# Kernel tuning notes

Measured on AMD Instinct MI355X. Metric: run time of the kernel, lower is better.

The kernel has to match this reference:

```python
import jax, jax.numpy as jnp
import numpy as np

B, H, W, C = 2, 128, 128, 256
WS = 8            # current_window (query window)
KW = 16           # halo_window = 2*current_window
HEADS = 8
HD = C // HEADS
PRETRAIN = 8
CPB_HIDDEN = 512


def _rel_bias_consts():
    halo = (KW - WS) // 2
    coords = np.arange(1 - WS - halo, WS + halo, dtype=np.float32)  # length WS+KW-1 = 23
    tab = np.stack(np.meshgrid(coords, coords, indexing='ij'), axis=-1)  # [23,23,2]
    tab = tab * (8.0 / (PRETRAIN - 1.0))
    tab = np.sign(tab) * np.log1p(np.abs(tab)) / np.log(8.0)
    tab = tab.reshape(-1, 2).astype(np.float32)                      # [529,2]
    qi = np.arange(WS)
    qg = np.stack(np.meshgrid(qi, qi, indexing='ij')).reshape(2, -1)  # [2,64]
    ki = np.arange(KW)
    kg = np.stack(np.meshgrid(ki, ki, indexing='ij')).reshape(2, -1)  # [2,256]
    rel = qg[:, :, None] - kg[:, None] + (KW - 1)
    idx = (rel[0] * (WS + KW - 1) + rel[1]).reshape(-1).astype(np.int32)  # [64*256]
    return tab, idx

_REL_TAB, _REL_IDX = _rel_bias_consts()


def setup_inputs() -> dict:
    key = jax.random.key(0)
    ks = jax.random.split(key, 12)
    s = 0.02
    return {
        'x': jax.random.normal(ks[0], (B, H, W, C), jnp.float32),
        'w_qkv': jax.random.normal(ks[1], (C, 3 * C), jnp.float32) * s,
        'w_dw': jax.random.normal(ks[2], (3, 3, 1, 3 * C), jnp.float32) * s,  # depthwise HWIO
        'ln_g': jnp.ones((3 * C,), jnp.float32),
        'ln_b': jnp.zeros((3 * C,), jnp.float32),
        'q_bias': jnp.zeros((C,), jnp.float32),
        'v_bias': jnp.zeros((C,), jnp.float32),
        'logit_scale': jnp.full((HEADS, 1, 1), np.log(10.0), jnp.float32),
        'cpb_w1': jax.random.normal(ks[3], (2, CPB_HIDDEN), jnp.float32) * s,
        'cpb_b1': jnp.zeros((CPB_HIDDEN,), jnp.float32),
        'cpb_w2': jax.random.normal(ks[4], (CPB_HIDDEN, HEADS), jnp.float32) * s,
        'w_proj': jax.random.normal(ks[5], (C, C), jnp.float32) * s,
    }


def _l2n(t):
    # tf.math.l2_normalize with epsilon=1.55e-5
    return t * jax.lax.rsqrt(jnp.maximum(jnp.sum(t * t, -1, keepdims=True), 1.55e-5))


def reference(x, w_qkv, w_dw, ln_g, ln_b, q_bias, v_bias, logit_scale,
              cpb_w1, cpb_b1, cpb_w2, w_proj):
    nWh, nWw = H // WS, W // WS
    nW = nWh * nWw
    # qkv 1x1 conv + depthwise 3x3 + layernorm + (q,0,v) bias
    qkv = jnp.einsum('bhwc,cd->bhwd', x, w_qkv)
    qkv = jax.lax.conv_general_dilated(
        qkv, w_dw, (1, 1), 'SAME',
        dimension_numbers=('NHWC', 'HWIO', 'NHWC'), feature_group_count=3 * C)
    mu = jnp.mean(qkv, -1, keepdims=True)
    var = jnp.var(qkv, -1, keepdims=True)
    qkv = (qkv - mu) * jax.lax.rsqrt(var + 1e-5) * ln_g + ln_b
    qkv = qkv + jnp.concatenate([q_bias, jnp.zeros_like(q_bias), v_bias])
    q, kv = qkv[..., :C], qkv[..., C:]
    # window partition of q: [B*nW, heads, WS*WS, HD]
    qp = q.reshape(B, nWh, WS, nWw, WS, HEADS, HD)
    qp = qp.transpose(0, 1, 3, 5, 2, 4, 6).reshape(B * nW, HEADS, WS * WS, HD)
    # halo partition of kv: overlapping KWxKW patches, stride WS
    halo = (KW - WS) // 2
    kvp = jnp.pad(kv, ((0, 0), (halo, halo), (halo, halo), (0, 0)))
    ridx = (np.arange(nWh) * WS)[:, None] + np.arange(KW)[None]  # [nWh,KW]
    cidx = (np.arange(nWw) * WS)[:, None] + np.arange(KW)[None]  # [nWw,KW]
    kvp = kvp[:, ridx][:, :, :, cidx]               # [B,nWh,KW,nWw,KW,2C]
    kvp = kvp.transpose(0, 1, 3, 2, 4, 5).reshape(B * nW, KW * KW, 2, HEADS, HD)
    k = kvp[:, :, 0].transpose(0, 2, 1, 3)          # [B*nW, heads, KW*KW, HD]
    v = kvp[:, :, 1].transpose(0, 2, 1, 3)
    # cosine attention with clamped learned log-scale
    scale = jnp.exp(jnp.minimum(logit_scale, np.float32(np.log(100.0))))
    attn = jnp.einsum('whqd,whkd->whqk', _l2n(qp) * scale, _l2n(k))
    # continuous relative position bias (CPB MLP + gather)
    hidden = jax.nn.relu(jnp.asarray(_REL_TAB) @ cpb_w1 + cpb_b1)
    bias_tab = jax.nn.sigmoid(hidden @ cpb_w2) * 16.0        # [529, heads]
    rb = bias_tab[_REL_IDX].reshape(WS * WS, KW * KW, HEADS).transpose(2, 0, 1)
    attn = jax.nn.softmax(attn + rb[None], axis=-1)
    out = jnp.einsum('whqk,whkd->whqd', attn, v)             # [B*nW, heads, 64, HD]
    # reverse window partition
    out = out.reshape(B, nWh, nWw, HEADS, WS, WS, HD)
    out = out.transpose(0, 1, 4, 2, 5, 3, 6).reshape(B, H, W, C)
    return jnp.einsum('bhwc,cd->bhwd', out, w_proj)
```

## Files before the change

kernel.cpp:

```cpp
#include <hip/hip_runtime.h>
#include <hip/hip_bf16.h>
#include <hip/hip_fp16.h>
#include <cstddef>
#include <cstdint>

#define BB 2
#define HH 128
#define WW 128
#define CC 256
#define WSZ 8
#define KWIN 16
#define NHEADS 8
#define HD 32
#define C3 768
#define NPIX 32768
#define NWIN 512

typedef short    bf16x8 __attribute__((ext_vector_type(8)));
typedef _Float16 half8  __attribute__((ext_vector_type(8)));
typedef float    f32x4  __attribute__((ext_vector_type(4)));

#define LOG2E 1.4426950408889634f

#if __has_builtin(__builtin_amdgcn_exp2f)
#define EXP2(x) __builtin_amdgcn_exp2f(x)
#else
#define EXP2(x) __expf((x) * 0.6931471805599453f)
#endif

__device__ inline void gload_lds16(const _Float16* g, _Float16* l) {
    __builtin_amdgcn_global_load_lds(
        (const __attribute__((address_space(1))) unsigned int*)g,
        (__attribute__((address_space(3))) unsigned int*)l, 16, 0, 0);
}

__global__ __launch_bounds__(64) void cpb_kernel(const float* __restrict__ w1,
                                                 const float* __restrict__ b1,
                                                 const float* __restrict__ w2,
                                                 float* __restrict__ btab) {
    const int e = blockIdx.x;
    const int i = e / 23, j = e % 23;
    const float inv_log8 = 1.0f / logf(8.0f);
    float c0 = (float)(i - 11) * (8.0f / 7.0f);
    float c1 = (float)(j - 11) * (8.0f / 7.0f);
    float f0 = copysignf(log1pf(fabsf(c0)) * inv_log8, c0);
    float f1 = copysignf(log1pf(fabsf(c1)) * inv_log8, c1);

    const int t = threadIdx.x;
    float acc[8] = {0.f,0.f,0.f,0.f,0.f,0.f,0.f,0.f};
    for (int kk = 0; kk < 8; kk++) {
        int k = kk * 64 + t;
        float hid = f0 * w1[k] + f1 * w1[512 + k] + b1[k];
        hid = fmaxf(hid, 0.f);
        #pragma unroll
        for (int h = 0; h < 8; h++) acc[h] += hid * w2[k * 8 + h];
    }
    #pragma unroll
    for (int h = 0; h < 8; h++) {
        #pragma unroll
        for (int off = 32; off >= 1; off >>= 1) acc[h] += __shfl_xor(acc[h], off);
    }
    if (t < 8) {
        float v = acc[t];
        btab[e * 8 + t] = 16.0f / (1.0f + expf(-v));
    }
}

__global__ __launch_bounds__(256) void cvt_wdw(const float* __restrict__ src,
                                               _Float16* __restrict__ dst) {
    int i = blockIdx.x * 256 + threadIdx.x;
    if (i < 9 * C3) dst[i] = (_Float16)src[i];
}

__global__ __launch_bounds__(256) void transpose_cvt(const float* __restrict__ src,
                                                     _Float16* __restrict__ dst,
                                                     int R, int Cn) {
    __shared__ float t[32][33];
    const int bx = blockIdx.x, by = blockIdx.y;
    const int tx = threadIdx.x & 31, ty = threadIdx.x >> 5;
    #pragma unroll
    for (int i = 0; i < 4; i++) {
        int r = by * 32 + ty + i * 8;
        t[ty + i * 8][tx] = src[(size_t)r * Cn + bx * 32 + tx];
    }
    __syncthreads();
    #pragma unroll
    for (int i = 0; i < 4; i++) {
        int dr = bx * 32 + ty + i * 8;
        dst[(size_t)dr * R + by * 32 + tx] = (_Float16)t[tx][ty + i * 8];
    }
}

template <typename OT>
__global__ __launch_bounds__(256) void gemm_f16(const _Float16* __restrict__ A,
                                                const _Float16* __restrict__ Bt,
                                                OT* __restrict__ C,
                                                int M, int N, int K) {
    __shared__ _Float16 Ash[128][64];
    __shared__ _Float16 Bsh[128][64];
    const int tid = threadIdx.x;
    const int wv = tid >> 6, ln = tid & 63;
    const int quad = ln >> 4, l15 = ln & 15;
    const int rowb = blockIdx.y * 128;
    const int colb = blockIdx.x * 128;
    const int wm = (wv >> 1) * 64, wn = (wv & 1) * 64;

    const int r8 = ln >> 3, g = ln & 7;
    const int kg = g ^ r8;

    f32x4 acc[4][4] = {};
    for (int k0 = 0; k0 < K; k0 += 64) {
        #pragma unroll
        for (int i = 0; i < 4; i++) {
            const int m = wv * 32 + i * 8 + r8;
            gload_lds16(A + (size_t)(rowb + m) * K + k0 + kg * 8,
                        &Ash[wv * 32 + i * 8][0]);
            gload_lds16(Bt + (size_t)(colb + m) * K + k0 + kg * 8,
                        &Bsh[wv * 32 + i * 8][0]);
        }
        __syncthreads();
        #pragma unroll
        for (int kk = 0; kk < 2; kk++) {
            const int phys = ((kk * 4 + quad) ^ (l15 & 7)) * 8;
            half8 a[4], b[4];
            #pragma unroll
            for (int i = 0; i < 4; i++)
                a[i] = *(const half8*)&Ash[wm + i * 16 + l15][phys];
            #pragma unroll
            for (int j = 0; j < 4; j++)
                b[j] = *(const half8*)&Bsh[wn + j * 16 + l15][phys];
            #pragma unroll
            for (int i = 0; i < 4; i++)
                #pragma unroll
                for (int j = 0; j < 4; j++)
                    acc[i][j] = __builtin_amdgcn_mfma_f32_16x16x32_f16(
                        a[i], b[j], acc[i][j], 0, 0, 0);
        }
        __syncthreads();
    }
    #pragma unroll
    for (int i = 0; i < 4; i++) {
        #pragma unroll
        for (int reg = 0; reg < 4; reg++) {
            const size_t row = rowb + wm + i * 16 + quad * 4 + reg;
            #pragma unroll
            for (int j = 0; j < 4; j++) {
                C[row * N + colb + wn + j * 16 + l15] = (OT)acc[i][j][reg];
            }
        }
    }
}

__global__ __launch_bounds__(256) void gemm_qkv(const float* __restrict__ A,
                                                const _Float16* __restrict__ Bt,
                                                _Float16* __restrict__ C,
                                                int M, int N, int K) {
    __shared__ _Float16 Ash[128][64];
    __shared__ _Float16 Bsh[128][64];
    const int tid = threadIdx.x;
    const int wv = tid >> 6, ln = tid & 63;
    const int quad = ln >> 4, l15 = ln & 15;
    const int rowb = blockIdx.y * 128;
    const int colb = blockIdx.x * 128;
    const int wm = (wv >> 1) * 64, wn = (wv & 1) * 64;
    const int r8 = ln >> 3, g = ln & 7;
    const int kg = g ^ r8;

    f32x4 acc[4][4] = {};
    for (int k0 = 0; k0 < K; k0 += 64) {
        #pragma unroll
        for (int i = 0; i < 4; i++) {
            const int m = wv * 32 + i * 8 + r8;
            const float* ap = A + (size_t)(rowb + m) * K + k0 + g * 8;
            const float4 a0 = *(const float4*)ap;
            const float4 a1 = *(const float4*)(ap + 4);
            half8 hv;
            hv[0] = (_Float16)a0.x; hv[1] = (_Float16)a0.y;
            hv[2] = (_Float16)a0.z; hv[3] = (_Float16)a0.w;
            hv[4] = (_Float16)a1.x; hv[5] = (_Float16)a1.y;
            hv[6] = (_Float16)a1.z; hv[7] = (_Float16)a1.w;
            *(half8*)&Ash[wv * 32 + i * 8 + r8][kg * 8] = hv;
            gload_lds16(Bt + (size_t)(colb + m) * K + k0 + kg * 8,
                        &Bsh[wv * 32 + i * 8][0]);
        }
        __syncthreads();
        #pragma unroll
        for (int kk = 0; kk < 2; kk++) {
            const int phys = ((kk * 4 + quad) ^ (l15 & 7)) * 8;
            half8 a[4], b[4];
            #pragma unroll
            for (int i = 0; i < 4; i++)
                a[i] = *(const half8*)&Ash[wm + i * 16 + l15][phys];
            #pragma unroll
            for (int j = 0; j < 4; j++)
                b[j] = *(const half8*)&Bsh[wn + j * 16 + l15][phys];
            #pragma unroll
            for (int i = 0; i < 4; i++)
                #pragma unroll
                for (int j = 0; j < 4; j++)
                    acc[i][j] = __builtin_amdgcn_mfma_f32_16x16x32_f16(
                        a[i], b[j], acc[i][j], 0, 0, 0);
        }
        __syncthreads();
    }
    #pragma unroll
    for (int i = 0; i < 4; i++) {
        #pragma unroll
        for (int reg = 0; reg < 4; reg++) {
            const size_t row = rowb + wm + i * 16 + quad * 4 + reg;
            #pragma unroll
            for (int j = 0; j < 4; j++) {
                C[row * N + colb + wn + j * 16 + l15] = (_Float16)acc[i][j][reg];
            }
        }
    }
}

__global__ __launch_bounds__(256) void dwconv_ln(const _Float16* __restrict__ in,
                                                 const _Float16* __restrict__ wdwh,
                                                 const float* __restrict__ g,
                                                 const float* __restrict__ bt,
                                                 const float* __restrict__ qb,
                                                 const float* __restrict__ vb,
                                                 _Float16* __restrict__ out) {
    __shared__ __align__(16) _Float16 S[2][960 * 8];
    __shared__ float sred[4][8][2];

    const int t = threadIdx.x;
    const int pix0 = blockIdx.x * 8;
    const int b = pix0 >> 14, y = (pix0 >> 7) & 127, x0 = pix0 & 127;
    const int p = t & 7, gidx = t >> 3;

    const _Float16* sp[4];
    int sphys[4];
    bool sok[4];
    #pragma unroll
    for (int k = 0; k < 4; k++) {
        const int u = t + k * 256;
        const int cell = u >> 5, grp = u & 31;
        const int r = (cell >= 20) ? 2 : (cell >= 10 ? 1 : 0);
        const int c = cell - r * 10;
        const int yy = y + r - 1, xx = x0 + c - 1;
        const bool inb = ((unsigned)yy < 128u) && ((unsigned)xx < 128u);
        sok[k] = inb;
        sp[k] = in + (((size_t)(b * 128 + (inb ? yy : 0)) * 128 + (inb ? xx : 0)) * C3)
                   + grp * 8;
        sphys[k] = (u & ~7) | ((u ^ c) & 7);
    }

    auto STAGE = [&](int s, int buf) {
        #pragma unroll
        for (int k = 0; k < 4; k++) {
            if (k < 3 || t < 192) {
                half8 v = (half8)(_Float16)0;
                if (sok[k]) v = *(const half8*)(sp[k] + s * 256);
                *(half8*)&S[buf][sphys[k] * 8] = v;
            }
        }
    };

    STAGE(0, 0);
    float acc[3][8] = {};
    #pragma unroll
    for (int s = 0; s < 3; s++) {
        __syncthreads();
        if (s < 2) STAGE(s + 1, (s + 1) & 1);
        const _Float16* Sb = &S[s & 1][0];
        half8 w[9];
        #pragma unroll
        for (int tap = 0; tap < 9; tap++)
            w[tap] = *(const half8*)(wdwh + (tap * 96 + s * 32 + gidx) * 8);
        #pragma unroll
        for (int r = 0; r < 3; r++) {
            #pragma unroll
            for (int dx = 0; dx < 3; dx++) {
                const int cc = p + dx;
                const int u = (r * 10 + cc) * 32 + gidx;
                const int phys = (u & ~7) | ((u ^ cc) & 7);
                const half8 v = *(const half8*)&Sb[phys * 8];
                const half8 wt = w[r * 3 + dx];
                #pragma unroll
                for (int i = 0; i < 8; i++)
                    acc[s][i] += (float)v[i] * (float)wt[i];
            }
        }
    }

    float ls = 0.f, lss = 0.f;
    #pragma unroll
    for (int s = 0; s < 3; s++)
        #pragma unroll
        for (int i = 0; i < 8; i++) { ls += acc[s][i]; lss += acc[s][i] * acc[s][i]; }
    ls  += __shfl_xor(ls, 8);  lss += __shfl_xor(lss, 8);
    ls  += __shfl_xor(ls, 16); lss += __shfl_xor(lss, 16);
    ls  += __shfl_xor(ls, 32); lss += __shfl_xor(lss, 32);
    const int wv = t >> 6, lnid = t & 63;
    if (lnid < 8) { sred[wv][lnid][0] = ls; sred[wv][lnid][1] = lss; }
    __syncthreads();
    const float Ssum  = sred[0][p][0] + sred[1][p][0] + sred[2][p][0] + sred[3][p][0];
    const float SSsum = sred[0][p][1] + sred[1][p][1] + sred[2][p][1] + sred[3][p][1];
    const float mu  = Ssum * (1.0f / 768.0f);
    const float var = SSsum * (1.0f / 768.0f) - mu * mu;
    const float rs  = rsqrtf(var + 1e-5f);

    const size_t obase = (size_t)(pix0 + p) * C3;
    #pragma unroll
    for (int s = 0; s < 3; s++) {
        const int ch = gidx * 8 + s * 256;
        const float4 g0 = *(const float4*)(g + ch);
        const float4 g1 = *(const float4*)(g + ch + 4);
        const float4 b0 = *(const float4*)(bt + ch);
        const float4 b1 = *(const float4*)(bt + ch + 4);
        float gg[8] = {g0.x, g0.y, g0.z, g0.w, g1.x, g1.y, g1.z, g1.w};
        float bb[8] = {b0.x, b0.y, b0.z, b0.w, b1.x, b1.y, b1.z, b1.w};
        if (s == 0) {
            const float4 e0 = *(const float4*)(qb + ch);
            const float4 e1 = *(const float4*)(qb + ch + 4);
            bb[0] += e0.x; bb[1] += e0.y; bb[2] += e0.z; bb[3] += e0.w;
            bb[4] += e1.x; bb[5] += e1.y; bb[6] += e1.z; bb[7] += e1.w;
        } else if (s == 2) {
            const float4 e0 = *(const float4*)(vb + ch - 512);
            const float4 e1 = *(const float4*)(vb + ch - 512 + 4);
            bb[0] += e0.x; bb[1] += e0.y; bb[2] += e0.z; bb[3] += e0.w;
            bb[4] += e1.x; bb[5] += e1.y; bb[6] += e1.z; bb[7] += e1.w;
        }
        half8 o;
        #pragma unroll
        for (int i = 0; i < 8; i++)
            o[i] = (_Float16)((acc[s][i] - mu) * rs * gg[i] + bb[i]);
        *(half8*)(out + obase + ch) = o;
    }
}

#define P2SHIFT 14.0f

__global__ __launch_bounds__(256) void attn_mfma(const _Float16* __restrict__ qkv,
                                                 const float* __restrict__ bias_tab,
                                                 const float* __restrict__ logit_scale,
                                                 _Float16* __restrict__ out) {
    const int blk = blockIdx.x;
    const int h = blk & 7;
    const int wid = blk >> 3;
    const int b = wid >> 8;
    const int wy = (wid >> 4) & 15;
    const int wx = wid & 15;
    const int tid = threadIdx.x;
    const int wave = tid >> 6, lane = tid & 63;
    const int quad = lane >> 4, l15 = lane & 15;

    __shared__ __align__(16) _Float16 Bf[16 * 64 * 8];
    __shared__ __align__(16) _Float16 Vt[32][264];
    __shared__ float btab[529];

    const float lscale = __expf(fminf(logit_scale[h], 4.60517019f));
    const float MshiftL2 = (lscale + 16.0f) * LOG2E - P2SHIFT;
    for (int e = tid; e < 529; e += 256)
        btab[e] = bias_tab[e * 8 + h] * LOG2E - MshiftL2;

    {
        const int j = tid;
        const int kr = j >> 4, kcc = j & 15;
        const int gy = wy * 8 - 4 + kr, gx = wx * 8 - 4 + kcc;
        const bool inb = ((unsigned)gy < 128u) && ((unsigned)gx < 128u);
        const _Float16* p = qkv +
            (((size_t)(b * 128 + (inb ? gy : 0)) * 128 + (inb ? gx : 0)) * C3) +
            256 + h * HD;
        float kreg[32];
        float s2 = 0.f;
        #pragma unroll
        for (int d8 = 0; d8 < 4; d8++) {
            half8 kk, vv;
            if (inb) { kk = *(const half8*)(p + d8 * 8); vv = *(const half8*)(p + 256 + d8 * 8); }
            else     { kk = (half8)(_Float16)0;          vv = (half8)(_Float16)0; }
            #pragma unroll
            for (int u = 0; u < 8; u++) {
                const float kf = (float)kk[u];
                kreg[d8 * 8 + u] = kf;
                s2 += kf * kf;
                Vt[d8 * 8 + u][j] = vv[u];
            }
        }
        const float r = rsqrtf(fmaxf(s2, 1.55e-5f));
        const int nt  = ((j >> 5) << 1) | ((j >> 2) & 1);
        const int pos = (((j >> 3) & 3) << 2) | (j & 3);
        #pragma unroll
        for (int d8 = 0; d8 < 4; d8++) {
            half8 hv;
            #pragma unroll
            for (int u = 0; u < 8; u++)
                hv[u] = (_Float16)(kreg[d8 * 8 + u] * r);
            *(half8*)&Bf[((nt * 64) + d8 * 16 + pos) * 8] = hv;
        }
    }

    const int qrow = wave * 16 + l15;
    const int qr = qrow >> 3, qc = qrow & 7;
    const int qy = wy * 8 + qr, qx = wx * 8 + qc;
    half8 qfrag;
    {
        const _Float16* qp = qkv + (((size_t)(b * 128 + qy) * 128 + qx) * C3) + h * HD + quad * 8;
        half8 q8 = *(const half8*)qp;
        float qf[8];
        float s2 = 0.f;
        #pragma unroll
        for (int u = 0; u < 8; u++) { qf[u] = (float)q8[u]; s2 += qf[u] * qf[u]; }
        s2 += __shfl_xor(s2, 16);
        s2 += __shfl_xor(s2, 32);
        const float rq = rsqrtf(fmaxf(s2, 1.55e-5f)) * lscale * LOG2E;
        #pragma unroll
        for (int u = 0; u < 8; u++) qfrag[u] = (_Float16)(qf[u] * rq);
    }
    __syncthreads();

    const int colbase = qc + 15 - ((quad & 1) << 3);
    const int rowq    = qr + 15 - (quad >> 1);
    float lsum = 0.f;
    f32x4 d0 = {0.f, 0.f, 0.f, 0.f};
    f32x4 d1 = {0.f, 0.f, 0.f, 0.f};
    #pragma unroll
    for (int ch = 0; ch < 8; ch++) {
        const half8 ka0 = *(const half8*)&Bf[((2 * ch)     * 64 + lane) * 8];
        const half8 ka1 = *(const half8*)&Bf[((2 * ch + 1) * 64 + lane) * 8];
        const float* bt = &btab[(rowq - 2 * ch) * 23 + colbase];
        f32x4 s0 = {bt[0],  bt[-1], bt[-2], bt[-3]};
        f32x4 s1 = {bt[-4], bt[-5], bt[-6], bt[-7]};
        __builtin_amdgcn_s_setprio(1);
        s0 = __builtin_amdgcn_mfma_f32_16x16x32_f16(ka0, qfrag, s0, 0, 0, 0);
        s1 = __builtin_amdgcn_mfma_f32_16x16x32_f16(ka1, qfrag, s1, 0, 0, 0);
        __builtin_amdgcn_s_setprio(0);
        half8 pa;
        #pragma unroll
        for (int r = 0; r < 4; r++) {
            const float p0 = EXP2(s0[r]);
            const float p1 = EXP2(s1[r]);
            lsum += p0 + p1;
            pa[r]     = (_Float16)p0;
            pa[4 + r] = (_Float16)p1;
        }
        const half8 v0 = *(const half8*)&Vt[l15][ch * 32 + quad * 8];
        const half8 v1 = *(const half8*)&Vt[l15 + 16][ch * 32 + quad * 8];
        __builtin_amdgcn_s_setprio(1);
        d0 = __builtin_amdgcn_mfma_f32_16x16x32_f16(pa, v0, d0, 0, 0, 0);
        d1 = __builtin_amdgcn_mfma_f32_16x16x32_f16(pa, v1, d1, 0, 0, 0);
        __builtin_amdgcn_s_setprio(0);
    }

    lsum += __shfl_xor(lsum, 16);
    lsum += __shfl_xor(lsum, 32);
    const float inv = 1.0f / lsum;

    #pragma unroll
    for (int reg = 0; reg < 4; reg++) {
        const int q = quad * 4 + reg;
        const float invq = __shfl(inv, q);
        const int gq = wave * 16 + q;
        const int oqr = gq >> 3, oqc = gq & 7;
        const int oy = wy * 8 + oqr, ox = wx * 8 + oqc;
        _Float16* op = out + (((size_t)(b * 128 + oy) * 128 + ox) * CC) + h * HD;
        op[l15]      = (_Float16)(d0[reg] * invq);
        op[16 + l15] = (_Float16)(d1[reg] * invq);
    }
}

extern "C" void kernel_launch(void* const* d_in, const int* in_sizes, int n_in,
                              void* d_out, int out_size, void* d_ws, size_t ws_size,
                              hipStream_t stream) {
    const float* x           = (const float*)d_in[0];
    const float* w_qkv       = (const float*)d_in[1];
    const float* w_dw        = (const float*)d_in[2];
    const float* ln_g        = (const float*)d_in[3];
    const float* ln_b        = (const float*)d_in[4];
    const float* q_bias      = (const float*)d_in[5];
    const float* v_bias      = (const float*)d_in[6];
    const float* logit_scale = (const float*)d_in[7];
    const float* cpb_w1      = (const float*)d_in[8];
    const float* cpb_b1      = (const float*)d_in[9];
    const float* cpb_w2      = (const float*)d_in[10];
    const float* w_proj      = (const float*)d_in[11];
    float* out = (float*)d_out;

    char* ws = (char*)d_ws;
    _Float16* attnh  = (_Float16*)(ws);
    _Float16* qkvh   = (_Float16*)(ws + 16777216);
    _Float16* qkv0h  = (_Float16*)(ws + 67108864);
    _Float16* wqkvT  = (_Float16*)(ws + 117440512);
    _Float16* wprojT = (_Float16*)(ws + 117833728);
    _Float16* wdwh   = (_Float16*)(ws + 117964800);
    float*    btab   = (float*)   (ws + 117981184);

    cpb_kernel<<<529, 64, 0, stream>>>(cpb_w1, cpb_b1, cpb_w2, btab);
    cvt_wdw<<<27, 256, 0, stream>>>(w_dw, wdwh);
    transpose_cvt<<<dim3(C3 / 32, CC / 32), 256, 0, stream>>>(w_qkv, wqkvT, CC, C3);
    transpose_cvt<<<dim3(CC / 32, CC / 32), 256, 0, stream>>>(w_proj, wprojT, CC, CC);

    gemm_qkv<<<dim3(C3 / 128, NPIX / 128), 256, 0, stream>>>(
        x, wqkvT, qkv0h, NPIX, C3, CC);
    dwconv_ln<<<NPIX / 8, 256, 0, stream>>>(qkv0h, wdwh, ln_g, ln_b, q_bias,
                                            v_bias, qkvh);
    attn_mfma<<<NWIN * NHEADS, 256, 0, stream>>>(qkvh, btab, logit_scale, attnh);
    gemm_f16<float><<<dim3(CC / 128, NPIX / 128), 256, 0, stream>>>(
        attnh, wprojT, out, NPIX, CC, CC);
}
```

Before: 241.3 us.

## Move q/k L2 normalization and logit scale into dwconv_ln epilogue, swizzle V layout

The per-head L2 normalization of q and k, plus the clamped logit scale applied to q, now happen in the dwconv+LayerNorm epilogue. Each head's sum of squares is reduced across the lanes holding its channels with shuffles. The attention kernel then loads q and k straight from memory without recomputing norms. This removes the normalization done 4x redundantly for every halo key across overlapping windows. The V transpose in shared memory is also changed to an XOR-swizzled fragment-ordered layout, intended to cut LDS bank conflicts on both the scattered writes and the half8 reads.

```diff
diff --git a/kernel.cpp b/kernel.cpp
--- a/kernel.cpp
+++ b/kernel.cpp
@@ -222,6 +222,7 @@
                                                  const float* __restrict__ bt,
                                                  const float* __restrict__ qb,
                                                  const float* __restrict__ vb,
+                                                 const float* __restrict__ logit_scale,
                                                  _Float16* __restrict__ out) {
     __shared__ __align__(16) _Float16 S[2][960 * 8];
     __shared__ float sred[4][8][2];
@@ -230,6 +231,8 @@
     const int pix0 = blockIdx.x * 8;
     const int b = pix0 >> 14, y = (pix0 >> 7) & 127, x0 = pix0 & 127;
     const int p = t & 7, gidx = t >> 3;
+
+    const float lsc_q = __expf(fminf(logit_scale[gidx >> 2], 4.60517019f)) * LOG2E;
 
     const _Float16* sp[4];
     int sphys[4];
@@ -324,10 +327,24 @@
             bb[0] += e0.x; bb[1] += e0.y; bb[2] += e0.z; bb[3] += e0.w;
             bb[4] += e1.x; bb[5] += e1.y; bb[6] += e1.z; bb[7] += e1.w;
         }
+        float of[8];
+        #pragma unroll
+        for (int i = 0; i < 8; i++)
+            of[i] = (acc[s][i] - mu) * rs * gg[i] + bb[i];
+        if (s < 2) {
+            float s2 = 0.f;
+            #pragma unroll
+            for (int i = 0; i < 8; i++) s2 += of[i] * of[i];
+            s2 += __shfl_xor(s2, 8);
+            s2 += __shfl_xor(s2, 16);
+            float scl = rsqrtf(fmaxf(s2, 1.55e-5f));
+            if (s == 0) scl *= lsc_q;
+            #pragma unroll
+            for (int i = 0; i < 8; i++) of[i] *= scl;
+        }
         half8 o;
         #pragma unroll
-        for (int i = 0; i < 8; i++)
-            o[i] = (_Float16)((acc[s][i] - mu) * rs * gg[i] + bb[i]);
+        for (int i = 0; i < 8; i++) o[i] = (_Float16)of[i];
         *(half8*)(out + obase + ch) = o;
     }
 }
@@ -349,7 +366,7 @@
     const int quad = lane >> 4, l15 = lane & 15;
 
     __shared__ __align__(16) _Float16 Bf[16 * 64 * 8];
-    __shared__ __align__(16) _Float16 Vt[32][264];
+    __shared__ __align__(16) _Float16 Vt2[1024 * 8];
     __shared__ float btab[529];
 
     const float lscale = __expf(fminf(logit_scale[h], 4.60517019f));
@@ -365,55 +382,35 @@
         const _Float16* p = qkv +
             (((size_t)(b * 128 + (inb ? gy : 0)) * 128 + (inb ? gx : 0)) * C3) +
             256 + h * HD;
-        float kreg[32];
-        float s2 = 0.f;
+        const int nt  = ((j >> 5) << 1) | ((j >> 2) & 1);
+        const int pos = (((j >> 3) & 3) << 2) | (j & 3);
+        const int ch_ = j >> 5, qq = (j >> 3) & 3, uu = j & 7;
+        const int swz = ((qq & 1) << 2) | ((ch_ & 1) << 1);
         #pragma unroll
         for (int d8 = 0; d8 < 4; d8++) {
             half8 kk, vv;
             if (inb) { kk = *(const half8*)(p + d8 * 8); vv = *(const half8*)(p + 256 + d8 * 8); }
             else     { kk = (half8)(_Float16)0;          vv = (half8)(_Float16)0; }
-            #pragma unroll
-            for (int u = 0; u < 8; u++) {
-                const float kf = (float)kk[u];
-                kreg[d8 * 8 + u] = kf;
-                s2 += kf * kf;
-                Vt[d8 * 8 + u][j] = vv[u];
+            *(half8*)&Bf[((nt * 64) + d8 * 16 + pos) * 8] = kk;
+            #pragma unroll
+            for (int u2 = 0; u2 < 8; u2++) {
+                const int d = d8 * 8 + u2;
+                const int unit = ((ch_ * 2 + (d >> 4)) * 64) + qq * 16 + ((d & 15) ^ swz);
+                Vt2[unit * 8 + uu] = vv[u2];
             }
-        }
-        const float r = rsqrtf(fmaxf(s2, 1.55e-5f));
-        const int nt  = ((j >> 5) << 1) | ((j >> 2) & 1);
-        const int pos = (((j >> 3) & 3) << 2) | (j & 3);
-        #pragma unroll
-        for (int d8 = 0; d8 < 4; d8++) {
-            half8 hv;
-            #pragma unroll
-            for (int u = 0; u < 8; u++)
-                hv[u] = (_Float16)(kreg[d8 * 8 + u] * r);
-            *(half8*)&Bf[((nt * 64) + d8 * 16 + pos) * 8] = hv;
         }
     }
 
     const int qrow = wave * 16 + l15;
     const int qr = qrow >> 3, qc = qrow & 7;
     const int qy = wy * 8 + qr, qx = wx * 8 + qc;
-    half8 qfrag;
-    {
-        const _Float16* qp = qkv + (((size_t)(b * 128 + qy) * 128 + qx) * C3) + h * HD + quad * 8;
-        half8 q8 = *(const half8*)qp;
-        float qf[8];
-        float s2 = 0.f;
-        #pragma unroll
-        for (int u = 0; u < 8; u++) { qf[u] = (float)q8[u]; s2 += qf[u] * qf[u]; }
-        s2 += __shfl_xor(s2, 16);
-        s2 += __shfl_xor(s2, 32);
-        const float rq = rsqrtf(fmaxf(s2, 1.55e-5f)) * lscale * LOG2E;
-        #pragma unroll
-        for (int u = 0; u < 8; u++) qfrag[u] = (_Float16)(qf[u] * rq);
-    }
+    const half8 qfrag = *(const half8*)(qkv +
+        (((size_t)(b * 128 + qy) * 128 + qx) * C3) + h * HD + quad * 8);
     __syncthreads();
 
     const int colbase = qc + 15 - ((quad & 1) << 3);
     const int rowq    = qr + 15 - (quad >> 1);
+    const int rsw     = (quad & 1) << 2;
     float lsum = 0.f;
     f32x4 d0 = {0.f, 0.f, 0.f, 0.f};
     f32x4 d1 = {0.f, 0.f, 0.f, 0.f};
@@ -437,8 +434,9 @@
             pa[r]     = (_Float16)p0;
             pa[4 + r] = (_Float16)p1;
         }
-        const half8 v0 = *(const half8*)&Vt[l15][ch * 32 + quad * 8];
-        const half8 v1 = *(const half8*)&Vt[l15 + 16][ch * 32 + quad * 8];
+        const int lsw = l15 ^ (rsw | ((ch & 1) << 1));
+        const half8 v0 = *(const half8*)&Vt2[(((ch * 2 + 0) * 64) + quad * 16 + lsw) * 8];
+        const half8 v1 = *(const half8*)&Vt2[(((ch * 2 + 1) * 64) + quad * 16 + lsw) * 8];
         __builtin_amdgcn_s_setprio(1);
         d0 = __builtin_amdgcn_mfma_f32_16x16x32_f16(pa, v0, d0, 0, 0, 0);
         d1 = __builtin_amdgcn_mfma_f32_16x16x32_f16(pa, v1, d1, 0, 0, 0);
@@ -496,7 +494,7 @@
     gemm_qkv<<<dim3(C3 / 128, NPIX / 128), 256, 0, stream>>>(
         x, wqkvT, qkv0h, NPIX, C3, CC);
     dwconv_ln<<<NPIX / 8, 256, 0, stream>>>(qkv0h, wdwh, ln_g, ln_b, q_bias,
-                                            v_bias, qkvh);
+                                            v_bias, logit_scale, qkvh);
     attn_mfma<<<NWIN * NHEADS, 256, 0, stream>>>(qkvh, btab, logit_scale, attnh);
     gemm_f16<float><<<dim3(CC / 128, NPIX / 128), 256, 0, stream>>>(
         attnh, wprojT, out, NPIX, CC, CC);
```

After: 240.3 us. No clear change (-0.4%).
